# Optimization experiments

Hardware: AMD Instinct MI355X
Metric: run time of the kernel (lower is better)

## Reference

```python
import jax, jax.numpy as jnp
import numpy as np

SOS = 4998
EOS = 4999
SCALING = 2.0


def setup_inputs() -> dict:
    key = jax.random.key(0)
    ks = jax.random.split(key, 12)
    B, T, E, D, A, C, F, ODIM, L = 32, 1000, 512, 1024, 512, 10, 100, 5000, 100
    s = 0.02
    return {
        "hpad": jax.random.normal(ks[0], (B, T, E), jnp.float32),
        "ys": jax.random.randint(ks[1], (B, L), 0, SOS, jnp.int32),
        # AttLoc params
        "w_enc": jax.random.normal(ks[2], (A, E), jnp.float32) * s,
        "b_enc": jnp.zeros((A,), jnp.float32),
        "w_dec": jax.random.normal(ks[3], (A, D), jnp.float32) * s,
        "w_att": jax.random.normal(ks[4], (A, C), jnp.float32) * s,
        "w_conv": jax.random.normal(ks[5], (C, 1, 2 * F + 1), jnp.float32) * s,  # OIH 1D conv kernel
        "w_gvec": jax.random.normal(ks[6], (1, A), jnp.float32) * s,
        "b_gvec": jnp.zeros((1,), jnp.float32),
        # Decoder params
        "embed": jax.random.normal(ks[7], (ODIM, D), jnp.float32) * s,
        "w_ih": jax.random.normal(ks[8], (4 * D, D + E), jnp.float32) * s,
        "w_hh": jax.random.normal(ks[9], (4 * D, D), jnp.float32) * s,
        "b_ih": jnp.zeros((4 * D,), jnp.float32),
        "b_hh": jnp.zeros((4 * D,), jnp.float32),
        "w_out": jax.random.normal(ks[10], (ODIM, D), jnp.float32) * s,
        "b_out": jnp.zeros((ODIM,), jnp.float32),
    }


def _decode(hpad, ys, w_enc, b_enc, w_dec, w_att, w_conv, w_gvec, b_gvec,
            embed, w_ih, w_hh, b_ih, b_hh, w_out, b_out):
    B, T, E = hpad.shape
    D = w_hh.shape[1]
    F = (w_conv.shape[-1] - 1) // 2
    # ys_in = [sos; y] per utterance (all same length -> already padded)
    ys_in = jnp.concatenate([jnp.full((B, 1), SOS, ys.dtype), ys], axis=1)  # [B, olen]
    eys = embed[ys_in]                                                      # [B, olen, D]
    # pre_compute_enc_h = mlp_enc(enc_h)
    pre = jnp.einsum('bte,ae->bta', hpad, w_enc) + b_enc                    # [B, T, A]
    att0 = jnp.full((B, T), 1.0 / T, hpad.dtype)   # uniform init attention (all hlen == T)
    z0 = jnp.zeros((B, D), hpad.dtype)
    c0 = jnp.zeros((B, D), hpad.dtype)

    def step(carry, ey_i):
        z, c, aw = carry
        # location-aware conv over previous attention weights: [B,1,T] -> [B,C,T]
        conv = jax.lax.conv_general_dilated(aw[:, None, :], w_conv, (1,), [(F, F)],
                                            dimension_numbers=('NCH', 'OIH', 'NCH'))
        att_feat = jnp.einsum('bct,ac->bta', conv, w_att)                   # mlp_att
        dec = (z @ w_dec.T)[:, None, :]                                     # mlp_dec, tiled
        e = jnp.tanh(att_feat + pre + dec) @ w_gvec[0] + b_gvec[0]          # [B, T]
        w = jax.nn.softmax(SCALING * e, axis=1)
        ctx = jnp.einsum('bt,bte->be', w, hpad)                             # [B, E]
        # LSTMCell
        x = jnp.concatenate([ey_i, ctx], axis=1)                            # [B, D+E]
        gates = x @ w_ih.T + b_ih + z @ w_hh.T + b_hh
        i_g, f_g, g_g, o_g = jnp.split(gates, 4, axis=1)
        c_new = jax.nn.sigmoid(f_g) * c + jax.nn.sigmoid(i_g) * jnp.tanh(g_g)
        z_new = jax.nn.sigmoid(o_g) * jnp.tanh(c_new)
        return (z_new, c_new, w), z_new

    _, z_all = jax.lax.scan(step, (z0, c0, att0), jnp.swapaxes(eys, 0, 1))  # [olen, B, D]
    y_all = jnp.einsum('obd,vd->obv', z_all, w_out) + b_out                 # [olen, B, odim]
    return jnp.swapaxes(y_all, 0, 1)                                        # [B, olen, odim]


def reference(hpad, ys, w_enc, b_enc, w_dec, w_att, w_conv, w_gvec, b_gvec,
              embed, w_ih, w_hh, b_ih, b_hh, w_out, b_out):
    return _decode(hpad, ys, w_enc, b_enc, w_dec, w_att, w_conv, w_gvec, b_gvec,
                   embed, w_ih, w_hh, b_ih, b_hh, w_out, b_out)
```

## Files before the change

kernel.cpp:

```cpp
#include <hip/hip_runtime.h>
#include <math.h>

#define B_    32
#define T_    1000
#define E_    512
#define D_    1024
#define A_    512
#define C_    10
#define F_    100
#define ODIM_ 5000
#define OLEN_ 101
#define SOS_  4998

#define OFF_PRE   0u
#define N_PREF    (32u*512u*1000u/2u)
#define OFF_HPB   (OFF_PRE + N_PREF)
#define N_HPBF    (32u*1000u*512u/2u)
#define OFF_PP    (OFF_HPB + N_HPBF)
#define N_PP      (32u*512u*12u)
#define OFF_CONV  (OFF_PP + N_PP)
#define N_CONVB   (32u*10u*1000u)
#define OFF_AW    (OFF_CONV + N_CONVB)
#define N_AW      (32u*1000u)
#define OFF_S     (OFF_AW + N_AW)
#define N_S       (64u)
#define OFF_CTX   (OFF_S + N_S)
#define N_CTX     (32u*512u)
#define OFF_GP    (OFF_CTX + N_CTX)
#define N_GP      (8u*32u*4096u)
#define OFF_Z     (OFF_GP + N_GP)
#define N_Z1      (32u*1024u)
#define OFF_C     (OFF_Z + N_Z1)
#define OFF_ZALL  (OFF_C + N_Z1)

__device__ __forceinline__ float fast_tanh(float x) {
    float cx = fminf(8.f, fmaxf(-8.f, x));
    float e = __expf(2.f * cx);
    return (e - 1.f) * __builtin_amdgcn_rcpf(e + 1.f);
}
__device__ __forceinline__ float fast_sigmoid(float x) {
    float cx = fminf(30.f, fmaxf(-30.f, x));
    return __builtin_amdgcn_rcpf(1.f + __expf(-cx));
}

__device__ __forceinline__ unsigned bf16rne(float f) {
    unsigned u = __float_as_uint(f);
    return (u + 0x7fffu + ((u >> 16) & 1u)) >> 16;
}
__device__ __forceinline__ unsigned packbf(float lo, float hi) {
    return bf16rne(lo) | (bf16rne(hi) << 16);
}
__device__ __forceinline__ float bflo(unsigned u) { return __uint_as_float(u << 16); }
__device__ __forceinline__ float bfhi(unsigned u) { return __uint_as_float(u & 0xffff0000u); }

__global__ __launch_bounds__(256) void k_init(const float* __restrict__ watt,
                                              const float* __restrict__ gvec,
                                              float* ws) {
    int i = blockIdx.x * 256 + threadIdx.x;
    if (i < (int)N_Z1) { ws[OFF_Z + i] = 0.f; ws[OFF_C + i] = 0.f; }
    if (i < (int)N_CTX) ws[OFF_CTX + i] = 0.f;
    if (i < (int)N_AW) ws[OFF_AW + i] = 1.0f;
    if (i < 64) ws[OFF_S + i] = (i >= 32) ? 1000.f : 0.f;
    if (i < 16384) {
        int a = i & 511;
        float* d = ws + OFF_PP + (size_t)i * 12;
        #pragma unroll
        for (int c = 0; c < 10; ++c) d[c] = watt[a * 10 + c];
        d[10] = gvec[a];
    }
}

__global__ __launch_bounds__(256) void k_hp16(const float* __restrict__ hp, float* ws) {
    uint2* hpb = (uint2*)(ws + OFF_HPB);
    const float4* src = (const float4*)hp;
    for (unsigned i = blockIdx.x * 256 + threadIdx.x; i < 4096000u; i += 4000u * 256u) {
        float4 v = src[i];
        uint2 o;
        o.x = packbf(v.x, v.y);
        o.y = packbf(v.z, v.w);
        hpb[i] = o;
    }
}

__global__ __launch_bounds__(256) void k_pre_t(const float* __restrict__ hp,
                                               const float* __restrict__ we,
                                               const float* __restrict__ be,
                                               float* ws) {
    __shared__ float As[64][68];
    __shared__ float Bs[64][68];
    unsigned short* preb = (unsigned short*)(ws + OFF_PRE);
    int bt = blockIdx.y;
    int b = bt >> 4, tc = bt & 15;
    int t0 = tc * 64;
    int n0 = blockIdx.x * 64;
    int tid = threadIdx.x;
    int tr = tid >> 4, tcl = tid & 15;
    float acc[4][4] = {};
    for (int k0 = 0; k0 < 512; k0 += 64) {
        for (int i = tid; i < 1024; i += 256) {
            int m = i >> 4, kq = (i & 15) << 2;
            int t = t0 + m;
            float4 v = (t < 1000) ? *(const float4*)&hp[((size_t)(b * 1000 + t)) * 512 + k0 + kq]
                                  : make_float4(0.f, 0.f, 0.f, 0.f);
            As[kq + 0][m] = v.x; As[kq + 1][m] = v.y; As[kq + 2][m] = v.z; As[kq + 3][m] = v.w;
            float4 w = *(const float4*)&we[(size_t)(n0 + m) * 512 + k0 + kq];
            Bs[kq + 0][m] = w.x; Bs[kq + 1][m] = w.y; Bs[kq + 2][m] = w.z; Bs[kq + 3][m] = w.w;
        }
        __syncthreads();
        #pragma unroll 16
        for (int kk = 0; kk < 64; ++kk) {
            float4 av = *(const float4*)&As[kk][tr << 2];
            float4 bv = *(const float4*)&Bs[kk][tcl << 2];
            float a[4] = {av.x, av.y, av.z, av.w};
            float bq[4] = {bv.x, bv.y, bv.z, bv.w};
            #pragma unroll
            for (int i = 0; i < 4; i++)
                #pragma unroll
                for (int j = 0; j < 4; j++) acc[i][j] += a[i] * bq[j];
        }
        __syncthreads();
    }
    int tt = t0 + (tr << 2);
    if (tt < 1000) {
        #pragma unroll
        for (int j = 0; j < 4; ++j) {
            int a = n0 + (tcl << 2) + j;
            float bea = be[a];
            uint2 o;
            o.x = packbf(acc[0][j] + bea, acc[1][j] + bea);
            o.y = packbf(acc[2][j] + bea, acc[3][j] + bea);
            *(uint2*)&preb[((size_t)(b * 512 + a)) * 1000 + tt] = o;
        }
    }
}

__global__ __launch_bounds__(256, 2) void k_prep(const float* __restrict__ wdec,
                                                 const float* __restrict__ wconv,
                                                 const float* __restrict__ wih,
                                                 const float* __restrict__ whh,
                                                 const float* __restrict__ embed,
                                                 const int* __restrict__ ys,
                                                 float* ws, int step) {
    int tid = threadIdx.x;
    if (blockIdx.x < 1024) {
        int u = blockIdx.x;
        if (u < 64) ws[OFF_CTX + u * 256 + tid] = 0.f;
        if (u == 64 && tid < 32) ws[OFF_S + (step & 1) * 32 + tid] = 0.f;
        int w = u * 4 + (tid >> 6);
        int lane = tid & 63;
        int a = w >> 3, bg7 = w & 7;
        const float4* wr = (const float4*)(wdec + (size_t)a * 1024);
        float4 w4[4];
        #pragma unroll
        for (int i = 0; i < 4; i++) w4[i] = wr[i * 64 + lane];
        float acc[4] = {0.f, 0.f, 0.f, 0.f};
        #pragma unroll
        for (int bb = 0; bb < 4; ++bb) {
            const float4* zr = (const float4*)(ws + OFF_Z + (size_t)(bg7 * 4 + bb) * 1024);
            #pragma unroll
            for (int i = 0; i < 4; i++) {
                float4 z4 = zr[i * 64 + lane];
                acc[bb] += w4[i].x * z4.x + w4[i].y * z4.y + w4[i].z * z4.z + w4[i].w * z4.w;
            }
        }
        #pragma unroll
        for (int off = 32; off > 0; off >>= 1) {
            acc[0] += __shfl_xor(acc[0], off, 64);
            acc[1] += __shfl_xor(acc[1], off, 64);
            acc[2] += __shfl_xor(acc[2], off, 64);
            acc[3] += __shfl_xor(acc[3], off, 64);
        }
        if (lane == 0) {
            #pragma unroll
            for (int bb = 0; bb < 4; ++bb)
                ws[OFF_PP + ((size_t)((bg7 * 4 + bb) * 512 + a)) * 12 + 11] = acc[bb];
        }
    } else if (blockIdx.x < 1344) {
        int blk = blockIdx.x - 1024;
        int b = blk / 10, c = blk - b * 10;
        if (tid >= 250) return;
        float invS = __builtin_amdgcn_rcpf(ws[OFF_S + ((step + 1) & 1) * 32 + b]);
        int t = tid * 4;
        const float* ar = ws + OFF_AW + b * 1000;
        const float* wc = wconv + c * 201;
        float a0, a1, a2, a3;
        a0 = (t - 100 >= 0) ? ar[t - 100] : 0.f;
        a1 = (t -  99 >= 0) ? ar[t -  99] : 0.f;
        a2 = (t -  98 >= 0) ? ar[t -  98] : 0.f;
        a3 = (t -  97 >= 0) ? ar[t -  97] : 0.f;
        float c0 = 0.f, c1 = 0.f, c2 = 0.f, c3 = 0.f;
        #pragma unroll 4
        for (int j = 0; j < 201; ++j) {
            float w = wc[j];
            c0 += a0 * w; c1 += a1 * w; c2 += a2 * w; c3 += a3 * w;
            a0 = a1; a1 = a2; a2 = a3;
            int ni = t + j - 96;
            a3 = (ni >= 0 && ni < 1000) ? ar[ni] : 0.f;
        }
        float* o = ws + OFF_CONV + (size_t)(b * 10 + c) * 1000 + t;
        o[0] = c0 * invS; o[1] = c1 * invS; o[2] = c2 * invS; o[3] = c3 * invS;
    } else {
        __shared__ float wlds[32][132];
        __shared__ float xs[32][36];
        int blk = blockIdx.x - 1344;
        int nt = blk & 31, ks = blk >> 5;
        int n0 = nt * 128;
        bool isE = (ks < 4);
        int kloc = isE ? ks * 256 : (ks - 4) * 256;
        int r = tid >> 1, h = tid & 1;
        int bx = tid >> 3, q8 = tid & 7;
        int tok = (step == 0) ? SOS_ : ys[bx * 100 + step - 1];
        const float* xsrc = isE ? (embed + (size_t)tok * 1024 + kloc)
                                : (ws + OFF_Z + (size_t)bx * 1024 + kloc);
        int nq = tid & 31, bq = tid >> 5;
        float acc[4][4] = {};
        for (int kc = 0; kc < 8; ++kc) {
            int koff = kc * 32;
            {
                const float* wrow = isE ? (wih + (size_t)(n0 + r) * 1536 + kloc + koff + h * 16)
                                        : (whh + (size_t)(n0 + r) * 1024 + kloc + koff + h * 16);
                #pragma unroll
                for (int j = 0; j < 4; ++j) {
                    float4 v = *(const float4*)&wrow[j * 4];
                    int kb = h * 16 + j * 4;
                    wlds[kb + 0][r] = v.x; wlds[kb + 1][r] = v.y;
                    wlds[kb + 2][r] = v.z; wlds[kb + 3][r] = v.w;
                }
            }
            {
                float4 v = *(const float4*)&xsrc[koff + q8 * 4];
                xs[q8 * 4 + 0][bx] = v.x; xs[q8 * 4 + 1][bx] = v.y;
                xs[q8 * 4 + 2][bx] = v.z; xs[q8 * 4 + 3][bx] = v.w;
            }
            __syncthreads();
            #pragma unroll 8
            for (int kk = 0; kk < 32; ++kk) {
                float4 wv = *(const float4*)&wlds[kk][nq * 4];
                float4 xv = *(const float4*)&xs[kk][bq * 4];
                float wa[4] = {wv.x, wv.y, wv.z, wv.w};
                float xa[4] = {xv.x, xv.y, xv.z, xv.w};
                #pragma unroll
                for (int i = 0; i < 4; i++)
                    #pragma unroll
                    for (int j = 0; j < 4; j++) acc[i][j] += wa[i] * xa[j];
            }
            __syncthreads();
        }
        float* gp = ws + OFF_GP + (size_t)(ks * 32 + bq * 4) * 4096 + n0 + nq * 4;
        #pragma unroll
        for (int j = 0; j < 4; j++)
            #pragma unroll
            for (int i = 0; i < 4; i++)
                gp[(size_t)j * 4096 + i] = acc[i][j];
    }
}

__global__ __launch_bounds__(512, 2) void k_ectx(const float* __restrict__ bgv,
                                                 float* ws, int step) {
    __shared__ float part[1024];
    __shared__ float wsh[128];
    const unsigned short* preb = (const unsigned short*)(ws + OFF_PRE);
    const unsigned short* hpb  = (const unsigned short*)(ws + OFF_HPB);
    int b = blockIdx.x >> 3, tc = blockIdx.x & 7;
    int tbase = tc * 128;
    int tid = threadIdx.x;
    int w = tid >> 6, l = tid & 63;
    int wu = __builtin_amdgcn_readfirstlane(w);
    int t = tbase + l * 2;
    bool valid = (t < 1000);
    float2 cvv[10];
    const float* convb = ws + OFF_CONV + b * 10000;
    #pragma unroll
    for (int c = 0; c < 10; ++c)
        cvv[c] = valid ? *(const float2*)&convb[c * 1000 + t] : make_float2(0.f, 0.f);
    const float* pb = ws + OFF_PP + ((size_t)(b * 512 + wu * 64)) * 12;
    const unsigned short* pt = preb + ((size_t)(b * 512 + wu * 64)) * 1000 + t;
    float ex = 0.f, ey = 0.f;
    #pragma unroll 8
    for (int i = 0; i < 64; ++i) {
        unsigned u = valid ? *(const unsigned*)pt : 0u;
        pt += 1000;
        float4 q0 = *(const float4*)(pb + i * 12);
        float4 q1 = *(const float4*)(pb + i * 12 + 4);
        float4 q2 = *(const float4*)(pb + i * 12 + 8);
        float px = bflo(u), py = bfhi(u);
        float sx = px + q2.w, sy = py + q2.w;
        sx += cvv[0].x * q0.x; sy += cvv[0].y * q0.x;
        sx += cvv[1].x * q0.y; sy += cvv[1].y * q0.y;
        sx += cvv[2].x * q0.z; sy += cvv[2].y * q0.z;
        sx += cvv[3].x * q0.w; sy += cvv[3].y * q0.w;
        sx += cvv[4].x * q1.x; sy += cvv[4].y * q1.x;
        sx += cvv[5].x * q1.y; sy += cvv[5].y * q1.y;
        sx += cvv[6].x * q1.z; sy += cvv[6].y * q1.z;
        sx += cvv[7].x * q1.w; sy += cvv[7].y * q1.w;
        sx += cvv[8].x * q2.x; sy += cvv[8].y * q2.x;
        sx += cvv[9].x * q2.y; sy += cvv[9].y * q2.y;
        ex += q2.z * fast_tanh(sx);
        ey += q2.z * fast_tanh(sy);
    }
    part[w * 128 + l * 2]     = ex;
    part[w * 128 + l * 2 + 1] = ey;
    __syncthreads();
    float wtil = 0.f;
    if (tid < 128) {
        int tt = tbase + tid;
        float e = 0.f;
        #pragma unroll
        for (int j = 0; j < 8; ++j) e += part[j * 128 + tid];
        if (tt < 1000) {
            wtil = __expf(2.f * (e + bgv[0]));
            ws[OFF_AW + b * 1000 + tt] = wtil;
        }
        wsh[tid] = wtil;
    }
    __syncthreads();
    if (tid < 128) {
        float ss = wtil;
        #pragma unroll
        for (int off = 32; off > 0; off >>= 1) ss += __shfl_xor(ss, off, 64);
        if ((tid & 63) == 0) part[tid >> 6] = ss;
    }
    __syncthreads();
    if (tid == 0) atomicAdd(&ws[OFF_S + (step & 1) * 32 + b], part[0] + part[1]);
    int e4 = tid & 127, th = tid >> 7;
    int lt0 = th * 32;
    int ltend = lt0 + 32;
    int tmax = 1000 - tbase; if (ltend > tmax) ltend = tmax;
    float4 acc = make_float4(0.f, 0.f, 0.f, 0.f);
    for (int lt = lt0; lt < ltend; ++lt) {
        float wv = wsh[lt];
        uint2 hu = *(const uint2*)&hpb[((size_t)(b * 1000 + tbase + lt)) * 512 + e4 * 4];
        acc.x += wv * bflo(hu.x); acc.y += wv * bfhi(hu.x);
        acc.z += wv * bflo(hu.y); acc.w += wv * bfhi(hu.y);
    }
    float* cx = ws + OFF_CTX + b * 512 + e4 * 4;
    atomicAdd(cx + 0, acc.x); atomicAdd(cx + 1, acc.y);
    atomicAdd(cx + 2, acc.z); atomicAdd(cx + 3, acc.w);
}

__global__ __launch_bounds__(256, 2) void k_gl(const float* __restrict__ wih,
                                               const float* __restrict__ bih,
                                               const float* __restrict__ bhh,
                                               float* ws, int step) {
    __shared__ float wlds[32][20];
    __shared__ float xs[32][33];
    __shared__ float glb[16][33];
    __shared__ float sinv[32];
    int tid = threadIdx.x;
    int d0 = blockIdx.x * 4;
    if (tid < 32) sinv[tid] = __builtin_amdgcn_rcpf(ws[OFF_S + (step & 1) * 32 + tid]);
    __syncthreads();
    int r = tid >> 4, h = tid & 15;
    int ng_r = (r >> 2) * 1024 + d0 + (r & 3);
    const float* wrow = wih + (size_t)ng_r * 1536 + 1024 + h * 2;
    int bx = tid >> 3, q8 = tid & 7;
    const float* xsrc = ws + OFF_CTX + (size_t)bx * 512 + q8 * 4;
    float xscale = sinv[bx];
    int nq = tid & 7, bq = tid >> 3;
    float acc[2] = {0.f, 0.f};
    for (int kc = 0; kc < 16; ++kc) {
        int k0 = kc * 32;
        {
            float2 v = *(const float2*)&wrow[k0];
            wlds[h * 2 + 0][r] = v.x;
            wlds[h * 2 + 1][r] = v.y;
        }
        {
            float4 v = *(const float4*)&xsrc[k0];
            xs[q8 * 4 + 0][bx] = v.x * xscale; xs[q8 * 4 + 1][bx] = v.y * xscale;
            xs[q8 * 4 + 2][bx] = v.z * xscale; xs[q8 * 4 + 3][bx] = v.w * xscale;
        }
        __syncthreads();
        #pragma unroll 8
        for (int kk = 0; kk < 32; ++kk) {
            float w0 = wlds[kk][nq * 2], w1 = wlds[kk][nq * 2 + 1];
            float x  = xs[kk][bq];
            acc[0] += w0 * x;
            acc[1] += w1 * x;
        }
        __syncthreads();
    }
    #pragma unroll
    for (int i = 0; i < 2; ++i) {
        int nl = nq * 2 + i;
        int ng = (nl >> 2) * 1024 + d0 + (nl & 3);
        float s = acc[i] + bih[ng] + bhh[ng];
        #pragma unroll
        for (int sl = 0; sl < 8; ++sl)
            s += ws[OFF_GP + (size_t)(sl * 32 + bq) * 4096 + ng];
        glb[nl][bq] = s;
    }
    __syncthreads();
    if (tid < 128) {
        int dl = tid >> 5, b = tid & 31;
        float gi = glb[dl][b];
        float gf = glb[4 + dl][b];
        float gg = glb[8 + dl][b];
        float go = glb[12 + dl][b];
        int id = b * 1024 + d0 + dl;
        float c_old = ws[OFF_C + id];
        float si = fast_sigmoid(gi);
        float sf = fast_sigmoid(gf);
        float so = fast_sigmoid(go);
        float cn = sf * c_old + si * fast_tanh(gg);
        float hh = so * fast_tanh(cn);
        ws[OFF_C + id] = cn;
        ws[OFF_Z + id] = hh;
        ws[OFF_ZALL + ((size_t)step * 32 + b) * 1024 + d0 + dl] = hh;
    }
}

__global__ __launch_bounds__(256) void k_out(const float* __restrict__ zall,
                                             const float* __restrict__ wo,
                                             const float* __restrict__ bo,
                                             float* __restrict__ out) {
    __shared__ float As[16][132];
    __shared__ float Bs[16][132];
    int m0 = blockIdx.y * 128, n0 = blockIdx.x * 128;
    int tid = threadIdx.x;
    int tx = tid & 15, ty = tid >> 4;
    float acc[8][8] = {};
    int ar = tid >> 1, ah = (tid & 1) * 8;
    for (int k0 = 0; k0 < 1024; k0 += 16) {
        {
            int gm = m0 + ar;
            float4 a0, a1;
            if (gm < 3232) {
                a0 = *(const float4*)&zall[(size_t)gm * 1024 + k0 + ah];
                a1 = *(const float4*)&zall[(size_t)gm * 1024 + k0 + ah + 4];
            } else { a0 = a1 = make_float4(0.f, 0.f, 0.f, 0.f); }
            As[ah + 0][ar] = a0.x; As[ah + 1][ar] = a0.y; As[ah + 2][ar] = a0.z; As[ah + 3][ar] = a0.w;
            As[ah + 4][ar] = a1.x; As[ah + 5][ar] = a1.y; As[ah + 6][ar] = a1.z; As[ah + 7][ar] = a1.w;
            int gn = n0 + ar;
            float4 b0, b1;
            if (gn < 5000) {
                b0 = *(const float4*)&wo[(size_t)gn * 1024 + k0 + ah];
                b1 = *(const float4*)&wo[(size_t)gn * 1024 + k0 + ah + 4];
            } else { b0 = b1 = make_float4(0.f, 0.f, 0.f, 0.f); }
            Bs[ah + 0][ar] = b0.x; Bs[ah + 1][ar] = b0.y; Bs[ah + 2][ar] = b0.z; Bs[ah + 3][ar] = b0.w;
            Bs[ah + 4][ar] = b1.x; Bs[ah + 5][ar] = b1.y; Bs[ah + 6][ar] = b1.z; Bs[ah + 7][ar] = b1.w;
        }
        __syncthreads();
        #pragma unroll
        for (int kk = 0; kk < 16; ++kk) {
            float4 a0v = *(const float4*)&As[kk][ty * 8];
            float4 a1v = *(const float4*)&As[kk][ty * 8 + 4];
            float4 b0v = *(const float4*)&Bs[kk][tx * 8];
            float4 b1v = *(const float4*)&Bs[kk][tx * 8 + 4];
            float am[8] = {a0v.x, a0v.y, a0v.z, a0v.w, a1v.x, a1v.y, a1v.z, a1v.w};
            float bn[8] = {b0v.x, b0v.y, b0v.z, b0v.w, b1v.x, b1v.y, b1v.z, b1v.w};
            #pragma unroll
            for (int i = 0; i < 8; i++)
                #pragma unroll
                for (int j = 0; j < 8; j++) acc[i][j] += am[i] * bn[j];
        }
        __syncthreads();
    }
    #pragma unroll
    for (int i = 0; i < 8; i++) {
        int m = m0 + ty * 8 + i;
        if (m >= 3232) continue;
        int b = m & 31, o = m >> 5;
        #pragma unroll
        for (int j = 0; j < 8; j++) {
            int v = n0 + tx * 8 + j;
            if (v < 5000)
                out[((size_t)b * 101 + o) * 5000 + v] = acc[i][j] + bo[v];
        }
    }
}

extern "C" void kernel_launch(void* const* d_in, const int* in_sizes, int n_in,
                              void* d_out, int out_size, void* d_ws, size_t ws_size,
                              hipStream_t stream) {
    const float* hpad   = (const float*)d_in[0];
    const int*   ys     = (const int*)d_in[1];
    const float* w_enc  = (const float*)d_in[2];
    const float* b_enc  = (const float*)d_in[3];
    const float* w_dec  = (const float*)d_in[4];
    const float* w_att  = (const float*)d_in[5];
    const float* w_conv = (const float*)d_in[6];
    const float* w_gvec = (const float*)d_in[7];
    const float* b_gvec = (const float*)d_in[8];
    const float* embed  = (const float*)d_in[9];
    const float* w_ih   = (const float*)d_in[10];
    const float* w_hh   = (const float*)d_in[11];
    const float* b_ih   = (const float*)d_in[12];
    const float* b_hh   = (const float*)d_in[13];
    const float* w_out  = (const float*)d_in[14];
    const float* b_out  = (const float*)d_in[15];
    float* ws  = (float*)d_ws;
    float* out = (float*)d_out;

    k_init<<<128, 256, 0, stream>>>(w_att, w_gvec, ws);
    k_hp16<<<4000, 256, 0, stream>>>(hpad, ws);
    k_pre_t<<<dim3(8, 512), 256, 0, stream>>>(hpad, w_enc, b_enc, ws);

    for (int step = 0; step < OLEN_; ++step) {
        k_prep<<<1600, 256, 0, stream>>>(w_dec, w_conv, w_ih, w_hh, embed, ys, ws, step);
        k_ectx<<<256, 512, 0, stream>>>(b_gvec, ws, step);
        k_gl<<<256, 256, 0, stream>>>(w_ih, b_ih, b_hh, ws, step);
    }

    k_out<<<dim3(40, 26), 256, 0, stream>>>(ws + OFF_ZALL, w_out, b_out, out);
}
```

Before: 9.958 ms.

## Fuse location conv into attention kernel and tile decoder projection with split-K

The location-aware 1D convolution moves out of k_prep and into k_ectx. Each block now computes the conv for its 128-timestep window from a shared-memory halo of the previous attention weights, which removes the global conv buffer round trip. The w_dec·z projection becomes an LDS-tiled GEMM split across 4 K-chunks, and its partial sums go into padded per-row slots (stride 16) that the attention kernel adds together. Attention weights are double-buffered so that reading the previous step's weights does not race with writing the new ones. The change cuts k_prep's grid from 1600 to 272 blocks, at the cost of redundant conv work per block and extra shared memory in k_ectx.

```diff
diff --git a/kernel.cpp b/kernel.cpp
--- a/kernel.cpp
+++ b/kernel.cpp
@@ -17,11 +17,10 @@
 #define OFF_HPB   (OFF_PRE + N_PREF)
 #define N_HPBF    (32u*1000u*512u/2u)
 #define OFF_PP    (OFF_HPB + N_HPBF)
-#define N_PP      (32u*512u*12u)
-#define OFF_CONV  (OFF_PP + N_PP)
-#define N_CONVB   (32u*10u*1000u)
-#define OFF_AW    (OFF_CONV + N_CONVB)
-#define N_AW      (32u*1000u)
+#define N_PP      (32u*512u*16u)
+#define OFF_AW    (OFF_PP + N_PP)
+#define N_AW1     (32u*1000u)
+#define N_AW      (2u*N_AW1)
 #define OFF_S     (OFF_AW + N_AW)
 #define N_S       (64u)
 #define OFF_CTX   (OFF_S + N_S)
@@ -60,13 +59,14 @@
     if (i < (int)N_Z1) { ws[OFF_Z + i] = 0.f; ws[OFF_C + i] = 0.f; }
     if (i < (int)N_CTX) ws[OFF_CTX + i] = 0.f;
     if (i < (int)N_AW) ws[OFF_AW + i] = 1.0f;
-    if (i < 64) ws[OFF_S + i] = (i >= 32) ? 1000.f : 0.f;
+    if (i < 64) ws[OFF_S + i] = 1000.f;
     if (i < 16384) {
         int a = i & 511;
-        float* d = ws + OFF_PP + (size_t)i * 12;
+        float* d = ws + OFF_PP + (size_t)i * 16;
         #pragma unroll
         for (int c = 0; c < 10; ++c) d[c] = watt[a * 10 + c];
         d[10] = gvec[a];
+        d[11] = 0.f; d[12] = 0.f; d[13] = 0.f; d[14] = 0.f; d[15] = 0.f;
     }
 }
 
@@ -135,74 +135,18 @@
 }
 
 __global__ __launch_bounds__(256, 2) void k_prep(const float* __restrict__ wdec,
-                                                 const float* __restrict__ wconv,
                                                  const float* __restrict__ wih,
                                                  const float* __restrict__ whh,
                                                  const float* __restrict__ embed,
                                                  const int* __restrict__ ys,
                                                  float* ws, int step) {
+    __shared__ float wlds[32][132];
+    __shared__ float xs[32][36];
     int tid = threadIdx.x;
-    if (blockIdx.x < 1024) {
-        int u = blockIdx.x;
-        if (u < 64) ws[OFF_CTX + u * 256 + tid] = 0.f;
-        if (u == 64 && tid < 32) ws[OFF_S + (step & 1) * 32 + tid] = 0.f;
-        int w = u * 4 + (tid >> 6);
-        int lane = tid & 63;
-        int a = w >> 3, bg7 = w & 7;
-        const float4* wr = (const float4*)(wdec + (size_t)a * 1024);
-        float4 w4[4];
-        #pragma unroll
-        for (int i = 0; i < 4; i++) w4[i] = wr[i * 64 + lane];
-        float acc[4] = {0.f, 0.f, 0.f, 0.f};
-        #pragma unroll
-        for (int bb = 0; bb < 4; ++bb) {
-            const float4* zr = (const float4*)(ws + OFF_Z + (size_t)(bg7 * 4 + bb) * 1024);
-            #pragma unroll
-            for (int i = 0; i < 4; i++) {
-                float4 z4 = zr[i * 64 + lane];
-                acc[bb] += w4[i].x * z4.x + w4[i].y * z4.y + w4[i].z * z4.z + w4[i].w * z4.w;
-            }
-        }
-        #pragma unroll
-        for (int off = 32; off > 0; off >>= 1) {
-            acc[0] += __shfl_xor(acc[0], off, 64);
-            acc[1] += __shfl_xor(acc[1], off, 64);
-            acc[2] += __shfl_xor(acc[2], off, 64);
-            acc[3] += __shfl_xor(acc[3], off, 64);
-        }
-        if (lane == 0) {
-            #pragma unroll
-            for (int bb = 0; bb < 4; ++bb)
-                ws[OFF_PP + ((size_t)((bg7 * 4 + bb) * 512 + a)) * 12 + 11] = acc[bb];
-        }
-    } else if (blockIdx.x < 1344) {
-        int blk = blockIdx.x - 1024;
-        int b = blk / 10, c = blk - b * 10;
-        if (tid >= 250) return;
-        float invS = __builtin_amdgcn_rcpf(ws[OFF_S + ((step + 1) & 1) * 32 + b]);
-        int t = tid * 4;
-        const float* ar = ws + OFF_AW + b * 1000;
-        const float* wc = wconv + c * 201;
-        float a0, a1, a2, a3;
-        a0 = (t - 100 >= 0) ? ar[t - 100] : 0.f;
-        a1 = (t -  99 >= 0) ? ar[t -  99] : 0.f;
-        a2 = (t -  98 >= 0) ? ar[t -  98] : 0.f;
-        a3 = (t -  97 >= 0) ? ar[t -  97] : 0.f;
-        float c0 = 0.f, c1 = 0.f, c2 = 0.f, c3 = 0.f;
-        #pragma unroll 4
-        for (int j = 0; j < 201; ++j) {
-            float w = wc[j];
-            c0 += a0 * w; c1 += a1 * w; c2 += a2 * w; c3 += a3 * w;
-            a0 = a1; a1 = a2; a2 = a3;
-            int ni = t + j - 96;
-            a3 = (ni >= 0 && ni < 1000) ? ar[ni] : 0.f;
-        }
-        float* o = ws + OFF_CONV + (size_t)(b * 10 + c) * 1000 + t;
-        o[0] = c0 * invS; o[1] = c1 * invS; o[2] = c2 * invS; o[3] = c3 * invS;
-    } else {
-        __shared__ float wlds[32][132];
-        __shared__ float xs[32][36];
-        int blk = blockIdx.x - 1344;
+    if (blockIdx.x < 256) {
+        if (blockIdx.x < 64) ws[OFF_CTX + blockIdx.x * 256 + tid] = 0.f;
+        if (blockIdx.x == 64 && tid < 32) ws[OFF_S + (step & 1) * 32 + tid] = 0.f;
+        int blk = blockIdx.x;
         int nt = blk & 31, ks = blk >> 5;
         int n0 = nt * 128;
         bool isE = (ks < 4);
@@ -252,39 +196,118 @@
             #pragma unroll
             for (int i = 0; i < 4; i++)
                 gp[(size_t)j * 4096 + i] = acc[i][j];
-    }
-}
-
-__global__ __launch_bounds__(512, 2) void k_ectx(const float* __restrict__ bgv,
+    } else {
+        int blk = blockIdx.x - 256;
+        int nt = blk & 3, ks = blk >> 2;
+        int n0 = nt * 128;
+        int kloc = ks * 256;
+        int r = tid >> 1, h = tid & 1;
+        int bx = tid >> 3, q8 = tid & 7;
+        const float* xsrc = ws + OFF_Z + (size_t)bx * 1024 + kloc;
+        int nq = tid & 31, bq = tid >> 5;
+        float acc[4][4] = {};
+        for (int kc = 0; kc < 8; ++kc) {
+            int koff = kc * 32;
+            {
+                const float* wrow = wdec + (size_t)(n0 + r) * 1024 + kloc + koff + h * 16;
+                #pragma unroll
+                for (int j = 0; j < 4; ++j) {
+                    float4 v = *(const float4*)&wrow[j * 4];
+                    int kb = h * 16 + j * 4;
+                    wlds[kb + 0][r] = v.x; wlds[kb + 1][r] = v.y;
+                    wlds[kb + 2][r] = v.z; wlds[kb + 3][r] = v.w;
+                }
+            }
+            {
+                float4 v = *(const float4*)&xsrc[koff + q8 * 4];
+                xs[q8 * 4 + 0][bx] = v.x; xs[q8 * 4 + 1][bx] = v.y;
+                xs[q8 * 4 + 2][bx] = v.z; xs[q8 * 4 + 3][bx] = v.w;
+            }
+            __syncthreads();
+            #pragma unroll 8
+            for (int kk = 0; kk < 32; ++kk) {
+                float4 wv = *(const float4*)&wlds[kk][nq * 4];
+                float4 xv = *(const float4*)&xs[kk][bq * 4];
+                float wa[4] = {wv.x, wv.y, wv.z, wv.w};
+                float xa[4] = {xv.x, xv.y, xv.z, xv.w};
+                #pragma unroll
+                for (int i = 0; i < 4; i++)
+                    #pragma unroll
+                    for (int j = 0; j < 4; j++) acc[i][j] += wa[i] * xa[j];
+            }
+            __syncthreads();
+        }
+        #pragma unroll
+        for (int j = 0; j < 4; j++)
+            #pragma unroll
+            for (int i = 0; i < 4; i++) {
+                int b = bq * 4 + j, a = n0 + nq * 4 + i;
+                ws[OFF_PP + ((size_t)(b * 512 + a)) * 16 + 11 + ks] = acc[i][j];
+            }
+    }
+}
+
+__global__ __launch_bounds__(512, 2) void k_ectx(const float* __restrict__ wconv,
+                                                 const float* __restrict__ bgv,
                                                  float* ws, int step) {
     __shared__ float part[1024];
     __shared__ float wsh[128];
+    __shared__ float awn[332];
+    __shared__ float wcv[2016];
+    __shared__ float cls[1280];
     const unsigned short* preb = (const unsigned short*)(ws + OFF_PRE);
     const unsigned short* hpb  = (const unsigned short*)(ws + OFF_HPB);
     int b = blockIdx.x >> 3, tc = blockIdx.x & 7;
     int tbase = tc * 128;
     int tid = threadIdx.x;
+    const float* awprev = ws + OFF_AW + ((step + 1) & 1) * N_AW1;
+    float*       awcur  = ws + OFF_AW + (step & 1) * N_AW1;
+    if (tid < 332) {
+        float invS = __builtin_amdgcn_rcpf(ws[OFF_S + ((step + 1) & 1) * 32 + b]);
+        int g = tbase - 100 + tid;
+        awn[tid] = (g >= 0 && g < 1000) ? awprev[b * 1000 + g] * invS : 0.f;
+    }
+    for (int i = tid; i < 2010; i += 512) wcv[i] = wconv[i];
+    __syncthreads();
+    if (tid < 320) {
+        int c = tid >> 5, tq = tid & 31;
+        int base = tq * 4;
+        const float* wc = wcv + c * 201;
+        float a0 = awn[base], a1 = awn[base + 1], a2 = awn[base + 2], a3 = awn[base + 3];
+        float c0 = 0.f, c1 = 0.f, c2 = 0.f, c3 = 0.f;
+        #pragma unroll 4
+        for (int j = 0; j < 201; ++j) {
+            float w = wc[j];
+            c0 += a0 * w; c1 += a1 * w; c2 += a2 * w; c3 += a3 * w;
+            a0 = a1; a1 = a2; a2 = a3;
+            a3 = awn[base + 4 + j];
+        }
+        *(float4*)&cls[c * 128 + base] = make_float4(c0, c1, c2, c3);
+    }
+    __syncthreads();
     int w = tid >> 6, l = tid & 63;
     int wu = __builtin_amdgcn_readfirstlane(w);
     int t = tbase + l * 2;
     bool valid = (t < 1000);
     float2 cvv[10];
-    const float* convb = ws + OFF_CONV + b * 10000;
     #pragma unroll
     for (int c = 0; c < 10; ++c)
-        cvv[c] = valid ? *(const float2*)&convb[c * 1000 + t] : make_float2(0.f, 0.f);
-    const float* pb = ws + OFF_PP + ((size_t)(b * 512 + wu * 64)) * 12;
+        cvv[c] = valid ? make_float2(cls[c * 128 + l * 2], cls[c * 128 + l * 2 + 1])
+                       : make_float2(0.f, 0.f);
+    const float* pb = ws + OFF_PP + ((size_t)(b * 512 + wu * 64)) * 16;
     const unsigned short* pt = preb + ((size_t)(b * 512 + wu * 64)) * 1000 + t;
     float ex = 0.f, ey = 0.f;
     #pragma unroll 8
     for (int i = 0; i < 64; ++i) {
         unsigned u = valid ? *(const unsigned*)pt : 0u;
         pt += 1000;
-        float4 q0 = *(const float4*)(pb + i * 12);
-        float4 q1 = *(const float4*)(pb + i * 12 + 4);
-        float4 q2 = *(const float4*)(pb + i * 12 + 8);
+        float4 q0 = *(const float4*)(pb + i * 16);
+        float4 q1 = *(const float4*)(pb + i * 16 + 4);
+        float4 q2 = *(const float4*)(pb + i * 16 + 8);
+        float4 q3 = *(const float4*)(pb + i * 16 + 12);
+        float dec = q2.w + q3.x + q3.y + q3.z;
         float px = bflo(u), py = bfhi(u);
-        float sx = px + q2.w, sy = py + q2.w;
+        float sx = px + dec, sy = py + dec;
         sx += cvv[0].x * q0.x; sy += cvv[0].y * q0.x;
         sx += cvv[1].x * q0.y; sy += cvv[1].y * q0.y;
         sx += cvv[2].x * q0.z; sy += cvv[2].y * q0.z;
@@ -309,7 +332,7 @@
         for (int j = 0; j < 8; ++j) e += part[j * 128 + tid];
         if (tt < 1000) {
             wtil = __expf(2.f * (e + bgv[0]));
-            ws[OFF_AW + b * 1000 + tt] = wtil;
+            awcur[b * 1000 + tt] = wtil;
         }
         wsh[tid] = wtil;
     }
@@ -492,13 +515,13 @@
     float* ws  = (float*)d_ws;
     float* out = (float*)d_out;
 
-    k_init<<<128, 256, 0, stream>>>(w_att, w_gvec, ws);
+    k_init<<<256, 256, 0, stream>>>(w_att, w_gvec, ws);
     k_hp16<<<4000, 256, 0, stream>>>(hpad, ws);
     k_pre_t<<<dim3(8, 512), 256, 0, stream>>>(hpad, w_enc, b_enc, ws);
 
     for (int step = 0; step < OLEN_; ++step) {
-        k_prep<<<1600, 256, 0, stream>>>(w_dec, w_conv, w_ih, w_hh, embed, ys, ws, step);
-        k_ectx<<<256, 512, 0, stream>>>(b_gvec, ws, step);
+        k_prep<<<272, 256, 0, stream>>>(w_dec, w_ih, w_hh, embed, ys, ws, step);
+        k_ectx<<<256, 512, 0, stream>>>(w_conv, b_gvec, ws, step);
         k_gl<<<256, 256, 0, stream>>>(w_ih, b_ih, b_hh, ws, step);
     }
 
```

Measured after the change: 10.86 ms. +9.0%, slower.
